# Kernel tuning notes

Hardware: AMD Instinct MI355X
Metric: run time of the kernel (lower is better)

Reference implementation:

```python
import jax, jax.numpy as jnp
import numpy as np

N_NODES = 100000
N_EDGES = 800000
N_LABEL = 400000
IN_CH = 256
OUT_CH = 256
H1 = 128
H2 = 32


def setup_inputs() -> dict:
    key = jax.random.key(0)
    ks = jax.random.split(key, 12)
    x = jax.random.normal(ks[0], (N_NODES, IN_CH), dtype=jnp.float32)
    edge_index = jax.random.randint(ks[1], (2, N_EDGES), 0, N_NODES, dtype=jnp.int64)
    edge_label_index = jax.random.randint(ks[2], (2, N_LABEL), 0, N_NODES, dtype=jnp.int64)
    # GCNConv params (PyG: lin weight + bias)
    s = 1.0 / np.sqrt(IN_CH)
    W_gcn = jax.random.uniform(ks[3], (IN_CH, OUT_CH), minval=-s, maxval=s, dtype=jnp.float32)
    b_gcn = jnp.zeros((OUT_CH,), dtype=jnp.float32)
    def lin(kw, kb, fin, fout):
        bound = 1.0 / np.sqrt(fin)
        W = jax.random.uniform(kw, (fin, fout), minval=-bound, maxval=bound, dtype=jnp.float32)
        b = jax.random.uniform(kb, (fout,), minval=-bound, maxval=bound, dtype=jnp.float32)
        return W, b
    W1, b1 = lin(ks[4], ks[5], OUT_CH, H1)
    W2, b2 = lin(ks[6], ks[7], H1, H2)
    W3, b3 = lin(ks[8], ks[9], H2, 1)
    return {"x": x, "edge_index": edge_index, "edge_label_index": edge_label_index,
            "W_gcn": W_gcn, "b_gcn": b_gcn, "W1": W1, "b1": b1,
            "W2": W2, "b2": b2, "W3": W3, "b3": b3}


def _gcn_conv(x, edge_index, W, b):
    # x' = D^{-1/2} (A + I) D^{-1/2} (x W) + b   (PyG GCNConv defaults)
    n = x.shape[0]
    x = x @ W  # [N, out]
    loops = jnp.arange(n, dtype=edge_index.dtype)
    src = jnp.concatenate([edge_index[0], loops])  # messages flow src -> dst
    dst = jnp.concatenate([edge_index[1], loops])
    deg = jax.ops.segment_sum(jnp.ones_like(dst, dtype=x.dtype), dst, num_segments=n)
    dis = jnp.where(deg > 0, jax.lax.rsqrt(jnp.maximum(deg, 1.0)), 0.0)
    norm = dis[src] * dis[dst]  # [E+N]
    msgs = x[src] * norm[:, None]
    out = jax.ops.segment_sum(msgs, dst, num_segments=n)
    return out + b


def reference(x, edge_index, edge_label_index, W_gcn, b_gcn, W1, b1, W2, b2, W3, b3):
    h = _gcn_conv(x, edge_index, W_gcn, b_gcn)  # [N, out]
    d = h[edge_label_index[1]] - h[edge_label_index[0]]  # [E_q, out]
    d = jax.nn.relu(d @ W1 + b1)
    d = jax.nn.relu(d @ W2 + b2)
    prob = d @ W3 + b3  # [E_q, 1]
    return prob.reshape(-1)
```

## Files before the change

kernel.cpp:

```cpp
#include <hip/hip_runtime.h>

#define N_NODES 100000
#define N_EDGES 800000
#define N_LABEL 400000

typedef __attribute__((ext_vector_type(8))) short bf16x8;
typedef __attribute__((ext_vector_type(4))) float f32x4;
typedef unsigned int uint;
typedef unsigned short ushort;

__device__ __forceinline__ ushort f2bf(float f) {
    uint u = __float_as_uint(f);
    u += 0x7FFFu + ((u >> 16) & 1u);
    return (ushort)(u >> 16);
}
__device__ __forceinline__ uint pack2(ushort a, ushort b) {
    return (uint)a | ((uint)b << 16);
}

__global__ void k_zero2(int* __restrict__ a, int* __restrict__ b) {
    int i = blockIdx.x * 256 + threadIdx.x;
    if (i < N_NODES) { a[i] = 0; b[i] = 0; }
}

__global__ void k_count(const int* __restrict__ ei, int* __restrict__ cnt) {
    int e = blockIdx.x * 256 + threadIdx.x;
    if (e < N_EDGES) atomicAdd(&cnt[ei[N_EDGES + e]], 1);
}

__global__ void k_dis(const int* __restrict__ cnt, float* __restrict__ dis) {
    int i = blockIdx.x * 256 + threadIdx.x;
    if (i < N_NODES) dis[i] = rsqrtf((float)(cnt[i] + 1));
}

__global__ __launch_bounds__(1024) void k_bsum(const int* __restrict__ cnt,
                                               int* __restrict__ bsum) {
    __shared__ int red[1024];
    int t = threadIdx.x;
    int i = blockIdx.x * 1024 + t;
    red[t] = (i < N_NODES) ? cnt[i] : 0;
    __syncthreads();
    #pragma unroll
    for (int off = 512; off; off >>= 1) {
        if (t < off) red[t] += red[t + off];
        __syncthreads();
    }
    if (t == 0) bsum[blockIdx.x] = red[0];
}

__global__ void k_bscan(int* __restrict__ bsum, int nb) {
    __shared__ int s[128];
    int t = threadIdx.x;
    s[t] = (t < nb) ? bsum[t] : 0;
    __syncthreads();
    #pragma unroll
    for (int off = 1; off < 128; off <<= 1) {
        int v = (t >= off) ? s[t - off] : 0;
        __syncthreads();
        s[t] += v;
        __syncthreads();
    }
    if (t < nb) bsum[t] = t ? s[t - 1] : 0;
}

__global__ __launch_bounds__(1024) void k_rowptr(const int* __restrict__ cnt,
                                                 const int* __restrict__ bsum,
                                                 int* __restrict__ rowptr) {
    __shared__ int s[1024];
    int t = threadIdx.x;
    int i = blockIdx.x * 1024 + t;
    int v = (i < N_NODES) ? cnt[i] : 0;
    s[t] = v;
    __syncthreads();
    #pragma unroll
    for (int off = 1; off < 1024; off <<= 1) {
        int u = (t >= off) ? s[t - off] : 0;
        __syncthreads();
        s[t] += u;
        __syncthreads();
    }
    int excl = s[t] - v + bsum[blockIdx.x];
    if (i < N_NODES) rowptr[i] = excl;
    if (i == N_NODES - 1) rowptr[N_NODES] = excl + v;
}

__global__ void k_fill(const int* __restrict__ ei, const int* __restrict__ rowptr,
                       int* __restrict__ cursor, int* __restrict__ csr) {
    int e = blockIdx.x * 256 + threadIdx.x;
    if (e >= N_EDGES) return;
    int src = ei[e];
    int dst = ei[N_EDGES + e];
    int pos = rowptr[dst] + atomicAdd(&cursor[dst], 1);
    csr[pos] = src;
}

__global__ __launch_bounds__(256) void gemm_f32(
    const float* __restrict__ A, const float* __restrict__ B,
    float* __restrict__ C, int M, int N, int K,
    const float* __restrict__ rowscale) {
    __shared__ float As[2][16][132];
    __shared__ float Bs[2][16][132];

    const int tid = threadIdx.x;
    const int tx = tid & 15, ty = tid >> 4;
    const int m0 = blockIdx.x * 128, n0 = blockIdx.y * 128;

    const int ar = tid >> 2;
    const int ac = (tid & 3) * 4;
    const int bk = tid >> 5;
    const int bc = (tid & 31) * 4;

    float acc[8][8] = {};
    float4 va[2], vb[2];

    auto loadG = [&](int k0) {
        #pragma unroll
        for (int hh = 0; hh < 2; ++hh) {
            int row = m0 + ar + hh * 64;
            va[hh] = make_float4(0.f, 0.f, 0.f, 0.f);
            if (row < M) va[hh] = *(const float4*)&A[(size_t)row * K + k0 + ac];
            vb[hh] = *(const float4*)&B[(size_t)(k0 + bk + hh * 8) * N + n0 + bc];
        }
    };
    auto storeL = [&](int buf) {
        #pragma unroll
        for (int hh = 0; hh < 2; ++hh) {
            As[buf][ac + 0][ar + hh * 64] = va[hh].x;
            As[buf][ac + 1][ar + hh * 64] = va[hh].y;
            As[buf][ac + 2][ar + hh * 64] = va[hh].z;
            As[buf][ac + 3][ar + hh * 64] = va[hh].w;
            *(float4*)&Bs[buf][bk + hh * 8][bc] = vb[hh];
        }
    };

    loadG(0);
    storeL(0);
    __syncthreads();

    int cur = 0;
    for (int k0 = 16;; k0 += 16) {
        const bool last = (k0 >= K);
        if (!last) loadG(k0);

        #pragma unroll
        for (int kk = 0; kk < 16; ++kk) {
            const float4 a0 = *(const float4*)&As[cur][kk][ty * 8];
            const float4 a1 = *(const float4*)&As[cur][kk][ty * 8 + 4];
            const float4 b0 = *(const float4*)&Bs[cur][kk][tx * 8];
            const float4 b1 = *(const float4*)&Bs[cur][kk][tx * 8 + 4];
            const float aa[8] = {a0.x, a0.y, a0.z, a0.w, a1.x, a1.y, a1.z, a1.w};
            const float bb[8] = {b0.x, b0.y, b0.z, b0.w, b1.x, b1.y, b1.z, b1.w};
            #pragma unroll
            for (int i = 0; i < 8; ++i)
                #pragma unroll
                for (int j = 0; j < 8; ++j)
                    acc[i][j] = fmaf(aa[i], bb[j], acc[i][j]);
        }
        if (last) break;
        storeL(cur ^ 1);
        __syncthreads();
        cur ^= 1;
    }

    #pragma unroll
    for (int i = 0; i < 8; ++i) {
        int row = m0 + ty * 8 + i;
        if (row < M) {
            float s = rowscale ? rowscale[row] : 1.0f;
            float4 c0 = {acc[i][0] * s, acc[i][1] * s, acc[i][2] * s, acc[i][3] * s};
            float4 c1 = {acc[i][4] * s, acc[i][5] * s, acc[i][6] * s, acc[i][7] * s};
            *(float4*)&C[(size_t)row * N + n0 + tx * 8] = c0;
            *(float4*)&C[(size_t)row * N + n0 + tx * 8 + 4] = c1;
        }
    }
}

__global__ void k_wsplit(const float* __restrict__ Wf, ushort* __restrict__ Bh,
                         ushort* __restrict__ Bl) {
    int id = blockIdx.x * 256 + threadIdx.x;
    if (id >= 32768) return;
    int j = id & 7, l = (id >> 3) & 63, ct = (id >> 9) & 7, s = id >> 12;
    int k = s * 32 + (l >> 4) * 8 + j;
    int col = ct * 16 + (l & 15);
    float w = Wf[k * 128 + col];
    ushort h = f2bf(w);
    float hf = __uint_as_float(((uint)h) << 16);
    ushort lo = f2bf(w - hf);
    Bh[id] = h;
    Bl[id] = lo;
}

__global__ __launch_bounds__(256) void gemm_mfma(
    const float* __restrict__ x, const ushort* __restrict__ Bh,
    const ushort* __restrict__ Bl, const float* __restrict__ dis,
    float* __restrict__ qs) {
    __shared__ __align__(16) ushort Ah[4096], Al[4096], Bhs[4096], Bls[4096];

    const int tid = threadIdx.x;
    const int w = tid >> 6, lane = tid & 63;
    const int m0 = blockIdx.x * 128;
    const int srow = tid >> 3;
    const int skq = tid & 7;

    f32x4 acc[2][8];
    #pragma unroll
    for (int i = 0; i < 2; ++i)
        #pragma unroll
        for (int j = 0; j < 8; ++j)
            acc[i][j] = (f32x4){0.f, 0.f, 0.f, 0.f};

    float4 r0, r1, r2, r3;
    uint4 pb0, pb1, pc0, pc1;

    auto xload = [&](int s) {
        const int kc = s * 32 + skq * 4;
        int row;
        const float4 z = make_float4(0.f, 0.f, 0.f, 0.f);
        row = m0 + srow;       r0 = (row < N_NODES) ? *(const float4*)&x[(size_t)row * 256 + kc] : z;
        row = m0 + 32 + srow;  r1 = (row < N_NODES) ? *(const float4*)&x[(size_t)row * 256 + kc] : z;
        row = m0 + 64 + srow;  r2 = (row < N_NODES) ? *(const float4*)&x[(size_t)row * 256 + kc] : z;
        row = m0 + 96 + srow;  r3 = (row < N_NODES) ? *(const float4*)&x[(size_t)row * 256 + kc] : z;
    };
    auto bload = [&](int s) {
        const uint4* ph = (const uint4*)(Bh + s * 4096);
        const uint4* pl = (const uint4*)(Bl + s * 4096);
        pb0 = ph[tid * 2]; pb1 = ph[tid * 2 + 1];
        pc0 = pl[tid * 2]; pc1 = pl[tid * 2 + 1];
    };
    auto stageA = [&](int p, const float4& v) {
        const int off = ((p * 2 + (srow >> 4)) * 64 + (skq >> 1) * 16 + (srow & 15)) * 8
                        + (skq & 1) * 4;
        ushort h0 = f2bf(v.x), h1 = f2bf(v.y), h2 = f2bf(v.z), h3 = f2bf(v.w);
        *(uint2*)&Ah[off] = make_uint2(pack2(h0, h1), pack2(h2, h3));
        float l0 = v.x - __uint_as_float(((uint)h0) << 16);
        float l1 = v.y - __uint_as_float(((uint)h1) << 16);
        float l2 = v.z - __uint_as_float(((uint)h2) << 16);
        float l3 = v.w - __uint_as_float(((uint)h3) << 16);
        *(uint2*)&Al[off] = make_uint2(pack2(f2bf(l0), f2bf(l1)),
                                       pack2(f2bf(l2), f2bf(l3)));
    };

    xload(0);
    bload(0);

    for (int s = 0; s < 8; ++s) {
        if (s) __syncthreads();
        stageA(0, r0); stageA(1, r1); stageA(2, r2); stageA(3, r3);
        *(uint4*)&Bhs[tid * 16] = pb0; *(uint4*)&Bhs[tid * 16 + 8] = pb1;
        *(uint4*)&Bls[tid * 16] = pc0; *(uint4*)&Bls[tid * 16 + 8] = pc1;
        if (s < 7) { xload(s + 1); bload(s + 1); }
        __syncthreads();

        const bf16x8 ah0 = *(const bf16x8*)&Ah[((w * 2 + 0) * 64 + lane) * 8];
        const bf16x8 al0 = *(const bf16x8*)&Al[((w * 2 + 0) * 64 + lane) * 8];
        const bf16x8 ah1 = *(const bf16x8*)&Ah[((w * 2 + 1) * 64 + lane) * 8];
        const bf16x8 al1 = *(const bf16x8*)&Al[((w * 2 + 1) * 64 + lane) * 8];
        #pragma unroll
        for (int ct = 0; ct < 8; ++ct) {
            const bf16x8 bh = *(const bf16x8*)&Bhs[(ct * 64 + lane) * 8];
            const bf16x8 bl = *(const bf16x8*)&Bls[(ct * 64 + lane) * 8];
            acc[0][ct] = __builtin_amdgcn_mfma_f32_16x16x32_bf16(al0, bh, acc[0][ct], 0, 0, 0);
            acc[0][ct] = __builtin_amdgcn_mfma_f32_16x16x32_bf16(ah0, bl, acc[0][ct], 0, 0, 0);
            acc[0][ct] = __builtin_amdgcn_mfma_f32_16x16x32_bf16(ah0, bh, acc[0][ct], 0, 0, 0);
            acc[1][ct] = __builtin_amdgcn_mfma_f32_16x16x32_bf16(al1, bh, acc[1][ct], 0, 0, 0);
            acc[1][ct] = __builtin_amdgcn_mfma_f32_16x16x32_bf16(ah1, bl, acc[1][ct], 0, 0, 0);
            acc[1][ct] = __builtin_amdgcn_mfma_f32_16x16x32_bf16(ah1, bh, acc[1][ct], 0, 0, 0);
        }
    }

    #pragma unroll
    for (int rt = 0; rt < 2; ++rt) {
        #pragma unroll
        for (int j = 0; j < 4; ++j) {
            const int row = m0 + w * 32 + rt * 16 + (lane >> 4) * 4 + j;
            if (row < N_NODES) {
                const float sc = dis[row];
                #pragma unroll
                for (int ct = 0; ct < 8; ++ct)
                    qs[(size_t)row * 128 + ct * 16 + (lane & 15)] = acc[rt][ct][j] * sc;
            }
        }
    }
}

__global__ __launch_bounds__(256) void k_gather(
    const float* __restrict__ qs, const int* __restrict__ rowptr,
    const int* __restrict__ csr, const float* __restrict__ dis,
    float* __restrict__ p) {
    int node = blockIdx.x * 4 + (threadIdx.x >> 6);
    if (node >= N_NODES) return;
    int lane = threadIdx.x & 63;
    int beg = rowptr[node], end = rowptr[node + 1];
    float2 acc = *(const float2*)&qs[(size_t)node * 128 + lane * 2];
    int j = beg;
    for (; j + 8 <= end; j += 8) {
        int s0 = csr[j],     s1 = csr[j + 1], s2 = csr[j + 2], s3 = csr[j + 3];
        int s4 = csr[j + 4], s5 = csr[j + 5], s6 = csr[j + 6], s7 = csr[j + 7];
        float2 v0 = *(const float2*)&qs[(size_t)s0 * 128 + lane * 2];
        float2 v1 = *(const float2*)&qs[(size_t)s1 * 128 + lane * 2];
        float2 v2 = *(const float2*)&qs[(size_t)s2 * 128 + lane * 2];
        float2 v3 = *(const float2*)&qs[(size_t)s3 * 128 + lane * 2];
        float2 v4 = *(const float2*)&qs[(size_t)s4 * 128 + lane * 2];
        float2 v5 = *(const float2*)&qs[(size_t)s5 * 128 + lane * 2];
        float2 v6 = *(const float2*)&qs[(size_t)s6 * 128 + lane * 2];
        float2 v7 = *(const float2*)&qs[(size_t)s7 * 128 + lane * 2];
        acc.x += v0.x; acc.y += v0.y;  acc.x += v1.x; acc.y += v1.y;
        acc.x += v2.x; acc.y += v2.y;  acc.x += v3.x; acc.y += v3.y;
        acc.x += v4.x; acc.y += v4.y;  acc.x += v5.x; acc.y += v5.y;
        acc.x += v6.x; acc.y += v6.y;  acc.x += v7.x; acc.y += v7.y;
    }
    for (; j + 4 <= end; j += 4) {
        int s0 = csr[j], s1 = csr[j + 1], s2 = csr[j + 2], s3 = csr[j + 3];
        float2 v0 = *(const float2*)&qs[(size_t)s0 * 128 + lane * 2];
        float2 v1 = *(const float2*)&qs[(size_t)s1 * 128 + lane * 2];
        float2 v2 = *(const float2*)&qs[(size_t)s2 * 128 + lane * 2];
        float2 v3 = *(const float2*)&qs[(size_t)s3 * 128 + lane * 2];
        acc.x += v0.x; acc.y += v0.y;  acc.x += v1.x; acc.y += v1.y;
        acc.x += v2.x; acc.y += v2.y;  acc.x += v3.x; acc.y += v3.y;
    }
    for (; j < end; ++j) {
        int src = csr[j];
        float2 v = *(const float2*)&qs[(size_t)src * 128 + lane * 2];
        acc.x += v.x;
        acc.y += v.y;
    }
    float d = dis[node];
    float2 r = {acc.x * d, acc.y * d};
    *(float2*)&p[(size_t)node * 128 + lane * 2] = r;
}

__global__ __launch_bounds__(256, 4) void k_edge_mlp(
    const float* __restrict__ p, const int* __restrict__ eli,
    const float* __restrict__ b1, const float* __restrict__ W2,
    const float* __restrict__ b2, const float* __restrict__ W3,
    const float* __restrict__ b3, float* __restrict__ out) {
    __shared__ float st[4][2][128];

    const int tid = threadIdx.x;
    const int wave = tid >> 6, lane = tid & 63;
    const int o = lane & 31, kh = lane >> 5;

    float w2r[64];
    #pragma unroll
    for (int i = 0; i < 64; ++i)
        w2r[i] = W2[(kh * 64 + i) * 32 + o];
    #pragma unroll
    for (int i = 0; i < 64; ++i)
        asm volatile("" : "+v"(w2r[i]));

    const float b2r = b2[o];
    const float w3r = W3[o];
    const float b3r = b3[0];
    const float4 bb4 = *(const float4*)&b1[o * 4];

    const int e0 = (blockIdx.x * 4 + wave) * 16;

    #pragma unroll 2
    for (int g = 0; g < 8; ++g) {
        const int e = e0 + g * 2 + kh;
        const int src = eli[e];
        const int dst = eli[N_LABEL + e];
        const float4 pd = *(const float4*)&p[(size_t)dst * 128 + o * 4];
        const float4 ps = *(const float4*)&p[(size_t)src * 128 + o * 4];
        float4 tv;
        tv.x = fmaxf(pd.x - ps.x + bb4.x, 0.f);
        tv.y = fmaxf(pd.y - ps.y + bb4.y, 0.f);
        tv.z = fmaxf(pd.z - ps.z + bb4.z, 0.f);
        tv.w = fmaxf(pd.w - ps.w + bb4.w, 0.f);
        *(float4*)&st[wave][kh][o * 4] = tv;

        float acc0 = 0.f, acc1 = 0.f;
        #pragma unroll
        for (int i = 0; i < 64; i += 4) {
            const float4 t0 = *(const float4*)&st[wave][0][kh * 64 + i];
            const float4 t1 = *(const float4*)&st[wave][1][kh * 64 + i];
            acc0 = fmaf(t0.x, w2r[i + 0], acc0);
            acc0 = fmaf(t0.y, w2r[i + 1], acc0);
            acc0 = fmaf(t0.z, w2r[i + 2], acc0);
            acc0 = fmaf(t0.w, w2r[i + 3], acc0);
            acc1 = fmaf(t1.x, w2r[i + 0], acc1);
            acc1 = fmaf(t1.y, w2r[i + 1], acc1);
            acc1 = fmaf(t1.z, w2r[i + 2], acc1);
            acc1 = fmaf(t1.w, w2r[i + 3], acc1);
        }
        float a0 = acc0 + __shfl_xor(acc0, 32);
        float u0 = fmaxf(a0 + b2r, 0.f) * w3r;
        #pragma unroll
        for (int m = 16; m; m >>= 1) u0 += __shfl_xor(u0, m);
        float a1 = acc1 + __shfl_xor(acc1, 32);
        float u1 = fmaxf(a1 + b2r, 0.f) * w3r;
        #pragma unroll
        for (int m = 16; m; m >>= 1) u1 += __shfl_xor(u1, m);
        if (lane == 0) {
            out[e0 + g * 2 + 0] = u0 + b3r;
            out[e0 + g * 2 + 1] = u1 + b3r;
        }
    }
}

extern "C" void kernel_launch(void* const* d_in, const int* in_sizes, int n_in,
                              void* d_out, int out_size, void* d_ws, size_t ws_size,
                              hipStream_t stream) {
    const float* x   = (const float*)d_in[0];
    const int*   ei  = (const int*)d_in[1];
    const int*   eli = (const int*)d_in[2];
    const float* Wg  = (const float*)d_in[3];
    const float* W1  = (const float*)d_in[5];
    const float* b1  = (const float*)d_in[6];
    const float* W2  = (const float*)d_in[7];
    const float* b2  = (const float*)d_in[8];
    const float* W3  = (const float*)d_in[9];
    const float* b3  = (const float*)d_in[10];
    float* out = (float*)d_out;

    char* ws = (char*)d_ws;
    float*  dis    = (float*)(ws + 0);
    int*    cnt    = (int*)(ws + 524288);
    int*    cursor = (int*)(ws + 1048576);
    int*    rowptr = (int*)(ws + 1572864);
    int*    bsum   = (int*)(ws + 2000000);
    int*    csr    = (int*)(ws + 2097152);
    float*  Wf     = (float*)(ws + 6291456);
    ushort* Bh     = (ushort*)(ws + 6422528);
    ushort* Bl     = (ushort*)(ws + 6488064);
    float*  qs     = (float*)(ws + 8388608);
    float*  p      = (float*)(ws + 59588608);

    const int NB = (N_NODES + 1023) / 1024;

    k_zero2<<<(N_NODES + 255) / 256, 256, 0, stream>>>(cnt, cursor);
    k_count<<<(N_EDGES + 255) / 256, 256, 0, stream>>>(ei, cnt);
    k_dis<<<(N_NODES + 255) / 256, 256, 0, stream>>>(cnt, dis);
    k_bsum<<<NB, 1024, 0, stream>>>(cnt, bsum);
    k_bscan<<<1, 128, 0, stream>>>(bsum, NB);
    k_rowptr<<<NB, 1024, 0, stream>>>(cnt, bsum, rowptr);
    k_fill<<<(N_EDGES + 255) / 256, 256, 0, stream>>>(ei, rowptr, cursor, csr);

    gemm_f32<<<dim3(2, 1), 256, 0, stream>>>(Wg, W1, Wf, 256, 128, 256, nullptr);

    k_wsplit<<<128, 256, 0, stream>>>(Wf, Bh, Bl);

    gemm_mfma<<<(N_NODES + 127) / 128, 256, 0, stream>>>(x, Bh, Bl, dis, qs);

    k_gather<<<(N_NODES + 3) / 4, 256, 0, stream>>>(qs, rowptr, csr, dis, p);

    k_edge_mlp<<<N_LABEL / 64, 256, 0, stream>>>(p, eli, b1, W2, b2, W3, b3, out);
}
```

Baseline: 372.7 us.

## Run edge MLP second layer on MFMA with split-bf16 precision

Replaces the scalar FMA loop in the edge MLP's 128->32 layer with bf16 MFMA instructions. Activations and W2 are each split into high and low bf16 parts, and three MFMAs per tile keep near-fp32 accuracy. A new pre-pass kernel lays W2 out in MFMA fragment order. The change removes the VALU-heavy dot products and the 64-register weight cache, at the cost of extra conversion work and LDS staging.

```diff
diff --git a/kernel.cpp b/kernel.cpp
--- a/kernel.cpp
+++ b/kernel.cpp
@@ -188,6 +188,21 @@
     ushort lo = f2bf(w - hf);
     Bh[id] = h;
     Bl[id] = lo;
+}
+
+__global__ void k_w2split(const float* __restrict__ W2, ushort* __restrict__ W2h,
+                          ushort* __restrict__ W2l) {
+    int id = blockIdx.x * 256 + threadIdx.x;
+    if (id >= 4096) return;
+    int j = id & 7, l = (id >> 3) & 63, ct = (id >> 9) & 1, s = id >> 10;
+    int k = s * 32 + (l >> 4) * 8 + j;
+    int col = ct * 16 + (l & 15);
+    float w = W2[k * 32 + col];
+    ushort h = f2bf(w);
+    float hf = __uint_as_float(((uint)h) << 16);
+    ushort lo = f2bf(w - hf);
+    W2h[id] = h;
+    W2l[id] = lo;
 }
 
 __global__ __launch_bounds__(256) void gemm_mfma(
@@ -331,70 +346,81 @@
 
 __global__ __launch_bounds__(256, 4) void k_edge_mlp(
     const float* __restrict__ p, const int* __restrict__ eli,
-    const float* __restrict__ b1, const float* __restrict__ W2,
-    const float* __restrict__ b2, const float* __restrict__ W3,
-    const float* __restrict__ b3, float* __restrict__ out) {
-    __shared__ float st[4][2][128];
+    const float* __restrict__ b1, const ushort* __restrict__ W2h,
+    const ushort* __restrict__ W2l, const float* __restrict__ b2,
+    const float* __restrict__ W3, const float* __restrict__ b3,
+    float* __restrict__ out) {
+    __shared__ __align__(16) ushort sth[4][2048], stl[4][2048];
 
     const int tid = threadIdx.x;
     const int wave = tid >> 6, lane = tid & 63;
-    const int o = lane & 31, kh = lane >> 5;
-
-    float w2r[64];
-    #pragma unroll
-    for (int i = 0; i < 64; ++i)
-        w2r[i] = W2[(kh * 64 + i) * 32 + o];
-    #pragma unroll
-    for (int i = 0; i < 64; ++i)
-        asm volatile("" : "+v"(w2r[i]));
-
-    const float b2r = b2[o];
-    const float w3r = W3[o];
+    const int row = lane & 15;
+    const int s = lane >> 4;
+
+    const int e0 = (blockIdx.x * 4 + wave) * 16;
+    const int src = eli[e0 + row];
+    const int dst = eli[N_LABEL + e0 + row];
+    const float* prd = &p[(size_t)dst * 128 + s * 32];
+    const float* prs = &p[(size_t)src * 128 + s * 32];
+
+    bf16x8 w2h[4][2], w2l[4][2];
+    #pragma unroll
+    for (int ss = 0; ss < 4; ++ss)
+        #pragma unroll
+        for (int ct = 0; ct < 2; ++ct) {
+            w2h[ss][ct] = *(const bf16x8*)&W2h[((ss * 2 + ct) * 64 + lane) * 8];
+            w2l[ss][ct] = *(const bf16x8*)&W2l[((ss * 2 + ct) * 64 + lane) * 8];
+        }
+
+    #pragma unroll
+    for (int cc = 0; cc < 8; ++cc) {
+        const float4 pd = *(const float4*)&prd[cc * 4];
+        const float4 ps = *(const float4*)&prs[cc * 4];
+        const float4 bb = *(const float4*)&b1[s * 32 + cc * 4];
+        float t0 = fmaxf(pd.x - ps.x + bb.x, 0.f);
+        float t1 = fmaxf(pd.y - ps.y + bb.y, 0.f);
+        float t2 = fmaxf(pd.z - ps.z + bb.z, 0.f);
+        float t3 = fmaxf(pd.w - ps.w + bb.w, 0.f);
+        ushort h0 = f2bf(t0), h1 = f2bf(t1), h2 = f2bf(t2), h3 = f2bf(t3);
+        const int off = (s * 64 + (cc >> 1) * 16 + row) * 8 + (cc & 1) * 4;
+        *(uint2*)&sth[wave][off] = make_uint2(pack2(h0, h1), pack2(h2, h3));
+        float l0 = t0 - __uint_as_float(((uint)h0) << 16);
+        float l1 = t1 - __uint_as_float(((uint)h1) << 16);
+        float l2 = t2 - __uint_as_float(((uint)h2) << 16);
+        float l3 = t3 - __uint_as_float(((uint)h3) << 16);
+        *(uint2*)&stl[wave][off] = make_uint2(pack2(f2bf(l0), f2bf(l1)),
+                                              pack2(f2bf(l2), f2bf(l3)));
+    }
+
+    f32x4 acc[2];
+    acc[0] = (f32x4){0.f, 0.f, 0.f, 0.f};
+    acc[1] = (f32x4){0.f, 0.f, 0.f, 0.f};
+    #pragma unroll
+    for (int ss = 0; ss < 4; ++ss) {
+        const bf16x8 ah = *(const bf16x8*)&sth[wave][(ss * 64 + lane) * 8];
+        const bf16x8 al = *(const bf16x8*)&stl[wave][(ss * 64 + lane) * 8];
+        #pragma unroll
+        for (int ct = 0; ct < 2; ++ct) {
+            acc[ct] = __builtin_amdgcn_mfma_f32_16x16x32_bf16(al, w2h[ss][ct], acc[ct], 0, 0, 0);
+            acc[ct] = __builtin_amdgcn_mfma_f32_16x16x32_bf16(ah, w2l[ss][ct], acc[ct], 0, 0, 0);
+            acc[ct] = __builtin_amdgcn_mfma_f32_16x16x32_bf16(ah, w2h[ss][ct], acc[ct], 0, 0, 0);
+        }
+    }
+
+    const float b2a = b2[lane & 15];
+    const float b2b = b2[16 + (lane & 15)];
+    const float w3a = W3[lane & 15];
+    const float w3b = W3[16 + (lane & 15)];
     const float b3r = b3[0];
-    const float4 bb4 = *(const float4*)&b1[o * 4];
-
-    const int e0 = (blockIdx.x * 4 + wave) * 16;
-
-    #pragma unroll 2
-    for (int g = 0; g < 8; ++g) {
-        const int e = e0 + g * 2 + kh;
-        const int src = eli[e];
-        const int dst = eli[N_LABEL + e];
-        const float4 pd = *(const float4*)&p[(size_t)dst * 128 + o * 4];
-        const float4 ps = *(const float4*)&p[(size_t)src * 128 + o * 4];
-        float4 tv;
-        tv.x = fmaxf(pd.x - ps.x + bb4.x, 0.f);
-        tv.y = fmaxf(pd.y - ps.y + bb4.y, 0.f);
-        tv.z = fmaxf(pd.z - ps.z + bb4.z, 0.f);
-        tv.w = fmaxf(pd.w - ps.w + bb4.w, 0.f);
-        *(float4*)&st[wave][kh][o * 4] = tv;
-
-        float acc0 = 0.f, acc1 = 0.f;
-        #pragma unroll
-        for (int i = 0; i < 64; i += 4) {
-            const float4 t0 = *(const float4*)&st[wave][0][kh * 64 + i];
-            const float4 t1 = *(const float4*)&st[wave][1][kh * 64 + i];
-            acc0 = fmaf(t0.x, w2r[i + 0], acc0);
-            acc0 = fmaf(t0.y, w2r[i + 1], acc0);
-            acc0 = fmaf(t0.z, w2r[i + 2], acc0);
-            acc0 = fmaf(t0.w, w2r[i + 3], acc0);
-            acc1 = fmaf(t1.x, w2r[i + 0], acc1);
-            acc1 = fmaf(t1.y, w2r[i + 1], acc1);
-            acc1 = fmaf(t1.z, w2r[i + 2], acc1);
-            acc1 = fmaf(t1.w, w2r[i + 3], acc1);
-        }
-        float a0 = acc0 + __shfl_xor(acc0, 32);
-        float u0 = fmaxf(a0 + b2r, 0.f) * w3r;
-        #pragma unroll
-        for (int m = 16; m; m >>= 1) u0 += __shfl_xor(u0, m);
-        float a1 = acc1 + __shfl_xor(acc1, 32);
-        float u1 = fmaxf(a1 + b2r, 0.f) * w3r;
-        #pragma unroll
-        for (int m = 16; m; m >>= 1) u1 += __shfl_xor(u1, m);
-        if (lane == 0) {
-            out[e0 + g * 2 + 0] = u0 + b3r;
-            out[e0 + g * 2 + 1] = u1 + b3r;
-        }
+    #pragma unroll
+    for (int j = 0; j < 4; ++j) {
+        float v = fmaxf(acc[0][j] + b2a, 0.f) * w3a
+                + fmaxf(acc[1][j] + b2b, 0.f) * w3b;
+        v += __shfl_xor(v, 1);
+        v += __shfl_xor(v, 2);
+        v += __shfl_xor(v, 4);
+        v += __shfl_xor(v, 8);
+        if ((lane & 15) == 0) out[e0 + s * 4 + j] = v + b3r;
     }
 }
 
@@ -423,6 +449,8 @@
     float*  Wf     = (float*)(ws + 6291456);
     ushort* Bh     = (ushort*)(ws + 6422528);
     ushort* Bl     = (ushort*)(ws + 6488064);
+    ushort* W2h    = (ushort*)(ws + 6553600);
+    ushort* W2l    = (ushort*)(ws + 6561792);
     float*  qs     = (float*)(ws + 8388608);
     float*  p      = (float*)(ws + 59588608);
 
@@ -439,10 +467,11 @@
     gemm_f32<<<dim3(2, 1), 256, 0, stream>>>(Wg, W1, Wf, 256, 128, 256, nullptr);
 
     k_wsplit<<<128, 256, 0, stream>>>(Wf, Bh, Bl);
+    k_w2split<<<16, 256, 0, stream>>>(W2, W2h, W2l);
 
     gemm_mfma<<<(N_NODES + 127) / 128, 256, 0, stream>>>(x, Bh, Bl, dis, qs);
 
     k_gather<<<(N_NODES + 3) / 4, 256, 0, stream>>>(qs, rowptr, csr, dis, p);
 
-    k_edge_mlp<<<N_LABEL / 64, 256, 0, stream>>>(p, eli, b1, W2, b2, W3, b3, out);
-}
+    k_edge_mlp<<<N_LABEL / 64, 256, 0, stream>>>(p, eli, b1, W2h, W2l, b2, W3, b3, out);
+}
```

Measured after the change: 344.0 us. -7.7%, faster.
